# Optimization experiments

Hardware: AMD Instinct MI355X
Metric: run time of the kernel (lower is better)

## Reference

```python
import jax, jax.numpy as jnp
import numpy as np

B, T, H, V, C = 8192, 40, 128, 4450, 102

def setup_inputs() -> dict:
    key = jax.random.key(0)
    ks = jax.random.split(key, 9)
    s = 1.0 / np.sqrt(H)
    return {
        "input_ids": jax.random.randint(ks[0], (B, T), 0, V, dtype=jnp.int64),
        "emb_c": jax.random.normal(ks[1], (V, H), jnp.float32),
        "emb_a": jax.random.normal(ks[2], (V, H), jnp.float32),
        "W_ih": jax.random.uniform(ks[3], (3 * H, H), jnp.float32, -s, s),
        "W_hh": jax.random.uniform(ks[4], (3 * H, H), jnp.float32, -s, s),
        "b_ih": jax.random.uniform(ks[5], (3 * H,), jnp.float32, -s, s),
        "b_hh": jax.random.uniform(ks[6], (3 * H,), jnp.float32, -s, s),
        "W_cls": jax.random.uniform(ks[7], (C, H), jnp.float32, -s, s),
        "b_cls": jax.random.uniform(ks[8], (C,), jnp.float32, -s, s),
    }

def _gru_scan(x_seq, W_ih, W_hh, b_ih, b_hh):
    # x_seq: [T, B, H]; PyTorch GRU gate order: r, z, n
    h0 = jnp.zeros((x_seq.shape[1], H), x_seq.dtype)
    def step(h, x):
        gi = x @ W_ih.T + b_ih          # [B, 3H]
        gh = h @ W_hh.T + b_hh          # [B, 3H]
        i_r, i_z, i_n = jnp.split(gi, 3, axis=-1)
        h_r, h_z, h_n = jnp.split(gh, 3, axis=-1)
        r = jax.nn.sigmoid(i_r + h_r)
        z = jax.nn.sigmoid(i_z + h_z)
        n = jnp.tanh(i_n + r * h_n)
        h_new = (1.0 - z) * n + z * h
        return h_new, h_new
    _, hs = jax.lax.scan(step, h0, x_seq)
    return hs                            # [T, B, H]

def reference(input_ids, emb_c, emb_a, W_ih, W_hh, b_ih, b_hh, W_cls, b_cls):
    x_a = emb_a[input_ids].transpose(1, 0, 2)   # [T, B, H]
    x_c = emb_c[input_ids].transpose(1, 0, 2)
    ha = _gru_scan(x_a, W_ih, W_hh, b_ih, b_hh).transpose(1, 0, 2)  # [B, T, H]
    hc = _gru_scan(x_c, W_ih, W_hh, b_ih, b_hh).transpose(1, 0, 2)
    matrix = jnp.einsum('bth,bsh->bts', ha, ha)  # [B, T, T]
    A = jax.nn.softmax(matrix, axis=1)           # Softmax(dim=1) over 3D
    attn = A.transpose(0, 2, 1)                  # [B, T, T]
    # bmm(hc^T [B,H,T], attn).transpose -> out[b,s,h] = sum_t hc[b,t,h]*attn[b,t,s]
    out = jnp.einsum('bth,bts->bsh', hc, attn)   # [B, T, H]
    logits = out.reshape(-1, H) @ W_cls.T + b_cls  # [B*T, C]
    return jax.nn.softmax(logits, axis=1)
```

## Files before the change

### kernel.cpp

```cpp
#include <hip/hip_runtime.h>
#include <hip/hip_bf16.h>

#define BB 8192
#define TT 40
#define HH 128
#define CC 102
#define VV 4450

typedef __attribute__((ext_vector_type(8))) short short8;
typedef __attribute__((ext_vector_type(4))) float f4;

__device__ __forceinline__ float sigmoidf_(float x) { return 1.f / (1.f + __expf(-x)); }
__device__ __forceinline__ float tanhf_(float x) { float e = __expf(2.f * x); return 1.f - 2.f / (e + 1.f); }

__device__ __forceinline__ unsigned short f2bf(float x) {
    union { float f; unsigned u; } v; v.f = x;
    unsigned r = v.u + 0x7FFFu + ((v.u >> 16) & 1u);
    return (unsigned short)(r >> 16);
}
__device__ __forceinline__ float bf2f(unsigned short h) {
    union { float f; unsigned u; } v; v.u = ((unsigned)h) << 16; return v.f;
}
__device__ __forceinline__ short8 u4s8(uint4 v) { return *(short8*)&v; }

#define MFMA16(acc, a, b) acc = __builtin_amdgcn_mfma_f32_16x16x32_bf16(a, b, acc, 0, 0, 0)

__global__ __launch_bounds__(256) void prep_bf16split(const float* __restrict__ W,
                                                      unsigned short* __restrict__ hi,
                                                      unsigned short* __restrict__ lo, int n) {
    int i = blockIdx.x * 256 + threadIdx.x;
    if (i < n) {
        float x = W[i];
        unsigned short h = f2bf(x);
        hi[i] = h;
        lo[i] = f2bf(x - bf2f(h));
    }
}

__global__ __launch_bounds__(256) void prep_wcls(const float* __restrict__ W,
                                                 unsigned short* __restrict__ hi,
                                                 unsigned short* __restrict__ lo) {
    int i = blockIdx.x * 256 + threadIdx.x;
    if (i < 112 * HH) {
        int r = i >> 7;
        float x = (r < CC) ? W[i] : 0.f;
        unsigned short h = f2bf(x);
        hi[i] = h;
        lo[i] = f2bf(x - bf2f(h));
    }
}

__global__ __launch_bounds__(256) void prep_G_mfma(
    const float* __restrict__ emb_a, const float* __restrict__ emb_c,
    const unsigned short* __restrict__ WihH, const unsigned short* __restrict__ WihL,
    const float* __restrict__ b_ih, const float* __restrict__ b_hh,
    float* __restrict__ G)
{
    __shared__ uint4 se[2][32][16];

    const int tid = threadIdx.x;
    const int src = blockIdx.y;
    const float* emb = src ? emb_c : emb_a;
    const int v0 = blockIdx.x * 32;

    const int lane = tid & 63;
    const int w = tid >> 6;
    const int mcol = lane & 15;
    const int quad = lane >> 4;

#pragma unroll
    for (int i = 0; i < 4; ++i) {
        int task = tid + 256 * i;
        int row = task >> 5, q = task & 31;
        int v = v0 + row;
        float4 x = make_float4(0.f, 0.f, 0.f, 0.f);
        if (v < VV) x = ((const float4*)(emb + (size_t)v * HH))[q];
        unsigned short h0 = f2bf(x.x), h1 = f2bf(x.y), h2 = f2bf(x.z), h3 = f2bf(x.w);
        unsigned short l0 = f2bf(x.x - bf2f(h0)), l1 = f2bf(x.y - bf2f(h1));
        unsigned short l2 = f2bf(x.z - bf2f(h2)), l3 = f2bf(x.w - bf2f(h3));
        uint2 Hw, Lw;
        Hw.x = (unsigned)h0 | ((unsigned)h1 << 16); Hw.y = (unsigned)h2 | ((unsigned)h3 << 16);
        Lw.x = (unsigned)l0 | ((unsigned)l1 << 16); Lw.y = (unsigned)l2 | ((unsigned)l3 << 16);
        int phys = (q >> 1) ^ (row & 15);
        ((uint2*)&se[0][row][phys])[q & 1] = Hw;
        ((uint2*)&se[1][row][phys])[q & 1] = Lw;
    }

    float bias[6];
#pragma unroll
    for (int n6 = 0; n6 < 6; ++n6) {
        int c = w * 96 + n6 * 16 + mcol;
        bias[n6] = b_ih[c] + (c < 256 ? b_hh[c] : 0.f);
    }

    f4 acc[2][6];
#pragma unroll
    for (int mt = 0; mt < 2; ++mt)
#pragma unroll
        for (int n6 = 0; n6 < 6; ++n6) acc[mt][n6] = (f4){0.f, 0.f, 0.f, 0.f};

    __syncthreads();

#pragma unroll
    for (int kk = 0; kk < 4; ++kk) {
        uint4 bH[6], bL[6];
#pragma unroll
        for (int n6 = 0; n6 < 6; ++n6) {
            int rowc = w * 96 + n6 * 16 + mcol;
            bH[n6] = *((const uint4*)WihH + rowc * 16 + kk * 4 + quad);
            bL[n6] = *((const uint4*)WihL + rowc * 16 + kk * 4 + quad);
        }
#pragma unroll
        for (int mt = 0; mt < 2; ++mt) {
            int m = mt * 16 + mcol;
            int phys = (kk * 4 + quad) ^ mcol;
            short8 ah = u4s8(se[0][m][phys]);
            short8 al = u4s8(se[1][m][phys]);
#pragma unroll
            for (int n6 = 0; n6 < 6; ++n6) {
                MFMA16(acc[mt][n6], ah, u4s8(bH[n6]));
                MFMA16(acc[mt][n6], ah, u4s8(bL[n6]));
                MFMA16(acc[mt][n6], al, u4s8(bH[n6]));
            }
        }
    }

    float* gout = G + (size_t)src * VV * 384;
#pragma unroll
    for (int mt = 0; mt < 2; ++mt)
#pragma unroll
        for (int r = 0; r < 4; ++r) {
            int m = mt * 16 + quad * 4 + r;
            int v = v0 + m;
            if (v < VV) {
#pragma unroll
                for (int n6 = 0; n6 < 6; ++n6) {
                    int c = w * 96 + n6 * 16 + mcol;
                    gout[(size_t)v * 384 + c] = acc[mt][n6][r] + bias[n6];
                }
            }
        }
}

__global__ __launch_bounds__(512, 2) void gru_mfma(
    const int* __restrict__ ids, const float* __restrict__ G,
    const __hip_bfloat16* __restrict__ Whi, const __hip_bfloat16* __restrict__ Wlo,
    const float* __restrict__ b_hh, float* __restrict__ ha, float* __restrict__ hc)
{
    __shared__ uint4 sh[2][2][32][16];
    __shared__ int sids[32 * TT];

    const int tid = threadIdx.x;
    const int src = blockIdx.y;
    const int b0 = blockIdx.x * 32;
    const float* Gs = G + (size_t)src * VV * 384;
    float* hout = src ? hc : ha;

    const int lane = tid & 63;
    const int w = tid >> 6;
    const int nc0 = w * 16;
    const int mcol = lane & 15;
    const int quad = lane >> 4;

    for (int idx = tid; idx < 32 * TT; idx += 512)
        sids[idx] = ids[b0 * TT + idx];

    {
        uint4 z; z.x = z.y = z.z = z.w = 0u;
        uint4* p = &sh[0][0][0][0];
        for (int idx = tid; idx < 2 * 32 * 16; idx += 512) p[idx] = z;
    }

    short8 bh[3][4], bl[3][4];
#pragma unroll
    for (int g = 0; g < 3; ++g)
#pragma unroll
        for (int kk = 0; kk < 4; ++kk) {
            int row = g * 128 + nc0 + mcol;
            uint4 vh = *((const uint4*)Whi + row * 16 + kk * 4 + quad);
            uint4 vl = *((const uint4*)Wlo + row * 16 + kk * 4 + quad);
            bh[g][kk] = u4s8(vh);
            bl[g][kk] = u4s8(vl);
        }

    const float bhn = b_hh[256 + nc0 + mcol];
    const float* gbase = Gs + nc0 + mcol;

    f4 hreg[2];
    hreg[0] = (f4){0.f, 0.f, 0.f, 0.f};
    hreg[1] = (f4){0.f, 0.f, 0.f, 0.f};

    __syncthreads();

    float gc[3][2][4];
#pragma unroll
    for (int mt = 0; mt < 2; ++mt)
#pragma unroll
        for (int reg = 0; reg < 4; ++reg) {
            int m = mt * 16 + quad * 4 + reg;
            int id = sids[m * TT + 0];
            const float* gp = gbase + (size_t)id * 384;
            gc[0][mt][reg] = gp[0];
            gc[1][mt][reg] = gp[128];
            gc[2][mt][reg] = gp[256];
        }

    int buf = 0;
#pragma unroll 1
    for (int t = 0; t < TT; ++t) {
        f4 acc[3][2];
#pragma unroll
        for (int g = 0; g < 3; ++g)
#pragma unroll
            for (int mt = 0; mt < 2; ++mt) acc[g][mt] = (f4){0.f, 0.f, 0.f, 0.f};

#pragma unroll
        for (int mt = 0; mt < 2; ++mt)
#pragma unroll
            for (int kk = 0; kk < 4; ++kk) {
                int m = mt * 16 + mcol;
                int phys = (kk * 4 + quad) ^ mcol;
                uint4 avh = sh[buf][0][m][phys];
                uint4 avl = sh[buf][1][m][phys];
                short8 ah = u4s8(avh), al = u4s8(avl);
#pragma unroll
                for (int g = 0; g < 3; ++g) {
                    MFMA16(acc[g][mt], ah, bh[g][kk]);
                    MFMA16(acc[g][mt], ah, bl[g][kk]);
                    MFMA16(acc[g][mt], al, bh[g][kk]);
                }
            }

        const int nbuf = buf ^ 1;
        const int j = nc0 + mcol;
        const int s_slot = j >> 3;
        const int jb = j & 7;
#pragma unroll
        for (int mt = 0; mt < 2; ++mt) {
#pragma unroll
            for (int reg = 0; reg < 4; ++reg) {
                float rr = sigmoidf_(acc[0][mt][reg] + gc[0][mt][reg]);
                float zz = sigmoidf_(acc[1][mt][reg] + gc[1][mt][reg]);
                float nn = tanhf_(gc[2][mt][reg] + rr * (acc[2][mt][reg] + bhn));
                float hv = (1.f - zz) * nn + zz * hreg[mt][reg];
                hreg[mt][reg] = hv;

                int m = mt * 16 + quad * 4 + reg;
                hout[((size_t)(b0 + m) * TT + t) * HH + j] = hv;

                unsigned short hb = f2bf(hv);
                unsigned short lb = f2bf(hv - bf2f(hb));
                int phys = s_slot ^ (m & 15);
                ((unsigned short*)&sh[nbuf][0][m][phys])[jb] = hb;
                ((unsigned short*)&sh[nbuf][1][m][phys])[jb] = lb;
            }
        }

        if (t < TT - 1) {
#pragma unroll
            for (int mt = 0; mt < 2; ++mt)
#pragma unroll
                for (int reg = 0; reg < 4; ++reg) {
                    int m = mt * 16 + quad * 4 + reg;
                    int id = sids[m * TT + t + 1];
                    const float* gp = gbase + (size_t)id * 384;
                    gc[0][mt][reg] = gp[0];
                    gc[1][mt][reg] = gp[128];
                    gc[2][mt][reg] = gp[256];
                }
        }
        __syncthreads();
        buf ^= 1;
    }
}

#define AT_SHA     0
#define AT_SHA_LO  12288
#define AT_SHCT    24576
#define AT_SHCT_LO 40960
#define AT_SM      57344
#define AT_SW      66752
#define AT_SW_LO   72896
#define AT_PARTM   79040
#define AT_PARTD   79808
#define AT_SMX     80576
#define AT_SDI     80768
#define AT_TOTAL   80960

__global__ __launch_bounds__(256, 2) void attn_cls_mfma(
    const float* __restrict__ ha, const float* __restrict__ hc,
    const unsigned short* __restrict__ WcH, const unsigned short* __restrict__ WcL,
    const float* __restrict__ b_cls, float* __restrict__ out)
{
    __shared__ __attribute__((aligned(16))) char smem[AT_TOTAL];
    const int tid = threadIdx.x;
    const int lane = tid & 63;
    const int w = tid >> 6;
    const int quad = lane >> 4;
    const int col = lane & 15;
    const size_t b = blockIdx.x;

    float* sm    = (float*)(smem + AT_SM);
    float* slog  = (float*)(smem + AT_SM);
    float* partM = (float*)(smem + AT_PARTM);
    float* partD = (float*)(smem + AT_PARTD);
    float* sMX   = (float*)(smem + AT_SMX);
    float* sDI   = (float*)(smem + AT_SDI);

    const int ntc0 = (w < 3) ? w : 3;
    const int ntc1 = (w < 3) ? w + 4 : 3;
    uint4 bw[2][4][2];
    float bcv[2];
    {
        int nts[2] = {ntc0, ntc1};
#pragma unroll
        for (int which = 0; which < 2; ++which) {
            int row = nts[which] * 16 + col;
#pragma unroll
            for (int kk = 0; kk < 4; ++kk) {
                bw[which][kk][0] = *((const uint4*)WcH + row * 16 + kk * 4 + quad);
                bw[which][kk][1] = *((const uint4*)WcL + row * 16 + kk * 4 + quad);
            }
            bcv[which] = (row < CC) ? b_cls[row] : 0.f;
        }
    }

    {
        const float4* hab = (const float4*)(ha + b * TT * HH);
#pragma unroll
        for (int i = 0; i < 5; ++i) {
            int f4i = tid + 256 * i;
            int row = f4i >> 5, q = f4i & 31;
            float4 v = hab[f4i];
            unsigned short h0 = f2bf(v.x), h1 = f2bf(v.y), h2 = f2bf(v.z), h3 = f2bf(v.w);
            unsigned short l0 = f2bf(v.x - bf2f(h0)), l1 = f2bf(v.y - bf2f(h1));
            unsigned short l2 = f2bf(v.z - bf2f(h2)), l3 = f2bf(v.w - bf2f(h3));
            uint2 Hw, Lw;
            Hw.x = (unsigned)h0 | ((unsigned)h1 << 16); Hw.y = (unsigned)h2 | ((unsigned)h3 << 16);
            Lw.x = (unsigned)l0 | ((unsigned)l1 << 16); Lw.y = (unsigned)l2 | ((unsigned)l3 << 16);
            int phys = (q >> 1) ^ (row & 15);
            int off = row * 256 + phys * 16 + (q & 1) * 8;
            *(uint2*)(smem + AT_SHA + off) = Hw;
            *(uint2*)(smem + AT_SHA_LO + off) = Lw;
        }
        if (tid < 128) {
            int row = 40 + (tid >> 4), c = tid & 15;
            uint4 z; z.x = z.y = z.z = z.w = 0u;
            *(uint4*)(smem + AT_SHA + row * 256 + c * 16) = z;
            *(uint4*)(smem + AT_SHA_LO + row * 256 + c * 16) = z;
        }
        const float* hcb = hc + b * TT * HH;
        for (int task = tid; task < 640; task += 256) {
            int h = task & 127, c = task >> 7;
            unsigned short H8[8], L8[8];
#pragma unroll
            for (int jj = 0; jj < 8; ++jj) {
                float x = hcb[(c * 8 + jj) * HH + h];
                H8[jj] = f2bf(x);
                L8[jj] = f2bf(x - bf2f(H8[jj]));
            }
            uint4 Hq, Lq;
            Hq.x = (unsigned)H8[0] | ((unsigned)H8[1] << 16); Hq.y = (unsigned)H8[2] | ((unsigned)H8[3] << 16);
            Hq.z = (unsigned)H8[4] | ((unsigned)H8[5] << 16); Hq.w = (unsigned)H8[6] | ((unsigned)H8[7] << 16);
            Lq.x = (unsigned)L8[0] | ((unsigned)L8[1] << 16); Lq.y = (unsigned)L8[2] | ((unsigned)L8[3] << 16);
            Lq.z = (unsigned)L8[4] | ((unsigned)L8[5] << 16); Lq.w = (unsigned)L8[6] | ((unsigned)L8[7] << 16);
            int phys = c ^ (h & 7);
            *(uint4*)(smem + AT_SHCT + h * 128 + phys * 16) = Hq;
            *(uint4*)(smem + AT_SHCT_LO + h * 128 + phys * 16) = Lq;
        }
        for (int task = tid; task < 384; task += 256) {
            int h = task & 127, c = 5 + (task >> 7);
            int phys = c ^ (h & 7);
            uint4 z; z.x = z.y = z.z = z.w = 0u;
            *(uint4*)(smem + AT_SHCT + h * 128 + phys * 16) = z;
            *(uint4*)(smem + AT_SHCT_LO + h * 128 + phys * 16) = z;
        }
    }
    __syncthreads();

    if (w < 3) {
        const int mt = w;
        uint4 aH[4], aL[4];
#pragma unroll
        for (int kk = 0; kk < 4; ++kk) {
            int phys = (kk * 4 + quad) ^ col;
            int off = (mt * 16 + col) * 256 + phys * 16;
            aH[kk] = *(uint4*)(smem + AT_SHA + off);
            aL[kk] = *(uint4*)(smem + AT_SHA_LO + off);
        }
        f4 acc[3];
#pragma unroll
        for (int nt = 0; nt < 3; ++nt) acc[nt] = (f4){0.f, 0.f, 0.f, 0.f};
#pragma unroll
        for (int kk = 0; kk < 4; ++kk) {
            short8 ah = u4s8(aH[kk]), al = u4s8(aL[kk]);
#pragma unroll
            for (int nt = 0; nt < 3; ++nt) {
                int phys = (kk * 4 + quad) ^ col;
                int off = (nt * 16 + col) * 256 + phys * 16;
                short8 bH = u4s8(*(uint4*)(smem + AT_SHA + off));
                short8 bL = u4s8(*(uint4*)(smem + AT_SHA_LO + off));
                MFMA16(acc[nt], ah, bH);
                MFMA16(acc[nt], ah, bL);
                MFMA16(acc[nt], al, bH);
            }
        }
#pragma unroll
        for (int nt = 0; nt < 3; ++nt)
#pragma unroll
            for (int r = 0; r < 4; ++r)
                sm[(mt * 16 + quad * 4 + r) * 49 + nt * 16 + col] = acc[nt][r];
    }
    __syncthreads();

    if (tid < 160) {
        int t = tid >> 2, p = tid & 3;
        const float* row = sm + t * 49 + p * 10;
        float M = row[0];
#pragma unroll
        for (int i = 1; i < 10; ++i) M = fmaxf(M, row[i]);
        float D = 0.f;
#pragma unroll
        for (int i = 0; i < 10; ++i) D += __expf(row[i] - M);
        partM[t * 4 + p] = M;
        partD[t * 4 + p] = D;
    }
    __syncthreads();
    if (tid < 40) {
        float M = partM[tid * 4];
        M = fmaxf(M, partM[tid * 4 + 1]); M = fmaxf(M, partM[tid * 4 + 2]); M = fmaxf(M, partM[tid * 4 + 3]);
        float D = 0.f;
#pragma unroll
        for (int p = 0; p < 4; ++p) D += partD[tid * 4 + p] * __expf(partM[tid * 4 + p] - M);
        sMX[tid] = M;
        sDI[tid] = 1.f / D;
    }
    __syncthreads();

    for (int task = tid; task < 384; task += 256) {
        int s = task >> 3, c = task & 7;
        uint4 Hq, Lq;
        if (c >= 5) {
            Hq.x = Hq.y = Hq.z = Hq.w = 0u; Lq = Hq;
        } else {
            const float* srow = sm + s * 49 + c * 8;
            unsigned short H8[8], L8[8];
#pragma unroll
            for (int jj = 0; jj < 8; ++jj) {
                int t = c * 8 + jj;
                float wv = __expf(srow[jj] - sMX[t]) * sDI[t];
                H8[jj] = f2bf(wv);
                L8[jj] = f2bf(wv - bf2f(H8[jj]));
            }
            Hq.x = (unsigned)H8[0] | ((unsigned)H8[1] << 16); Hq.y = (unsigned)H8[2] | ((unsigned)H8[3] << 16);
            Hq.z = (unsigned)H8[4] | ((unsigned)H8[5] << 16); Hq.w = (unsigned)H8[6] | ((unsigned)H8[7] << 16);
            Lq.x = (unsigned)L8[0] | ((unsigned)L8[1] << 16); Lq.y = (unsigned)L8[2] | ((unsigned)L8[3] << 16);
            Lq.z = (unsigned)L8[4] | ((unsigned)L8[5] << 16); Lq.w = (unsigned)L8[6] | ((unsigned)L8[7] << 16);
        }
        int phys = c ^ (s & 7);
        *(uint4*)(smem + AT_SW + s * 128 + phys * 16) = Hq;
        *(uint4*)(smem + AT_SW_LO + s * 128 + phys * 16) = Lq;
    }
    __syncthreads();

    {
        uint4 aH[3][2], aL[3][2];
#pragma unroll
        for (int mt = 0; mt < 3; ++mt)
#pragma unroll
            for (int kk = 0; kk < 2; ++kk) {
                int s = mt * 16 + col;
                int phys = (kk * 4 + quad) ^ (s & 7);
                aH[mt][kk] = *(uint4*)(smem + AT_SW + s * 128 + phys * 16);
                aL[mt][kk] = *(uint4*)(smem + AT_SW_LO + s * 128 + phys * 16);
            }
        f4 acc[3][2];
#pragma unroll
        for (int mt = 0; mt < 3; ++mt) { acc[mt][0] = (f4){0,0,0,0}; acc[mt][1] = (f4){0,0,0,0}; }
#pragma unroll
        for (int which = 0; which < 2; ++which) {
            int nt = w + which * 4;
            int hrow = nt * 16 + col;
#pragma unroll
            for (int kk = 0; kk < 2; ++kk) {
                int phys = (kk * 4 + quad) ^ (hrow & 7);
                short8 bH = u4s8(*(uint4*)(smem + AT_SHCT + hrow * 128 + phys * 16));
                short8 bL = u4s8(*(uint4*)(smem + AT_SHCT_LO + hrow * 128 + phys * 16));
#pragma unroll
                for (int mt = 0; mt < 3; ++mt) {
                    short8 ah = u4s8(aH[mt][kk]), al = u4s8(aL[mt][kk]);
                    MFMA16(acc[mt][which], ah, bH);
                    MFMA16(acc[mt][which], ah, bL);
                    MFMA16(acc[mt][which], al, bH);
                }
            }
        }
        __syncthreads();
#pragma unroll
        for (int which = 0; which < 2; ++which) {
            int h = (w + which * 4) * 16 + col;
            int chunk = h >> 3, hb7 = (h & 7) * 2;
#pragma unroll
            for (int mt = 0; mt < 3; ++mt)
#pragma unroll
                for (int r = 0; r < 4; ++r) {
                    float v = acc[mt][which][r];
                    int s = mt * 16 + quad * 4 + r;
                    unsigned short hbv = f2bf(v);
                    unsigned short lbv = f2bf(v - bf2f(hbv));
                    int phys = chunk ^ (s & 15);
                    *(unsigned short*)(smem + AT_SHA + s * 256 + phys * 16 + hb7) = hbv;
                    *(unsigned short*)(smem + AT_SHA_LO + s * 256 + phys * 16 + hb7) = lbv;
                }
        }
    }
    __syncthreads();

    {
        f4 acc[3][2];
#pragma unroll
        for (int mt = 0; mt < 3; ++mt) { acc[mt][0] = (f4){0,0,0,0}; acc[mt][1] = (f4){0,0,0,0}; }
#pragma unroll
        for (int kk = 0; kk < 4; ++kk)
#pragma unroll
            for (int mt = 0; mt < 3; ++mt) {
                int s = mt * 16 + col;
                int phys = (kk * 4 + quad) ^ (s & 15);
                short8 ah = u4s8(*(uint4*)(smem + AT_SHA + s * 256 + phys * 16));
                short8 al = u4s8(*(uint4*)(smem + AT_SHA_LO + s * 256 + phys * 16));
#pragma unroll
                for (int which = 0; which < 2; ++which) {
                    MFMA16(acc[mt][which], ah, u4s8(bw[which][kk][0]));
                    MFMA16(acc[mt][which], ah, u4s8(bw[which][kk][1]));
                    MFMA16(acc[mt][which], al, u4s8(bw[which][kk][0]));
                }
            }
        __syncthreads();
        int nts[2] = {ntc0, ntc1};
#pragma unroll
        for (int which = 0; which < 2; ++which) {
            int c = nts[which] * 16 + col;
#pragma unroll
            for (int mt = 0; mt < 3; ++mt)
#pragma unroll
                for (int r = 0; r < 4; ++r)
                    slog[(mt * 16 + quad * 4 + r) * 113 + c] = acc[mt][which][r] + bcv[which];
        }
    }
    __syncthreads();

    if (tid < 160) {
        int s = tid >> 2, p = tid & 3;
        int c0 = p * 26;
        int c1 = (c0 + 26 < CC) ? c0 + 26 : CC;
        const float* row = slog + s * 113;
        float M = row[c0];
        for (int c = c0 + 1; c < c1; ++c) M = fmaxf(M, row[c]);
        float D = 0.f;
        for (int c = c0; c < c1; ++c) D += __expf(row[c] - M);
        partM[s * 4 + p] = M;
        partD[s * 4 + p] = D;
    }
    __syncthreads();
    if (tid < 40) {
        float M = partM[tid * 4];
        M = fmaxf(M, partM[tid * 4 + 1]); M = fmaxf(M, partM[tid * 4 + 2]); M = fmaxf(M, partM[tid * 4 + 3]);
        float D = 0.f;
#pragma unroll
        for (int p = 0; p < 4; ++p) D += partD[tid * 4 + p] * __expf(partM[tid * 4 + p] - M);
        sMX[tid] = M;
        sDI[tid] = 1.f / D;
    }
    __syncthreads();

    {
        int c = tid & 127, s0 = tid >> 7;
        if (c < CC) {
            float* ob = out + b * TT * CC;
            for (int s = s0; s < TT; s += 2)
                ob[s * CC + c] = __expf(slog[s * 113 + c] - sMX[s]) * sDI[s];
        }
    }
}

extern "C" void kernel_launch(void* const* d_in, const int* in_sizes, int n_in,
                              void* d_out, int out_size, void* d_ws, size_t ws_size,
                              hipStream_t stream) {
    const int*   ids   = (const int*)d_in[0];
    const float* emb_c = (const float*)d_in[1];
    const float* emb_a = (const float*)d_in[2];
    const float* W_ih  = (const float*)d_in[3];
    const float* W_hh  = (const float*)d_in[4];
    const float* b_ih  = (const float*)d_in[5];
    const float* b_hh  = (const float*)d_in[6];
    const float* W_cls = (const float*)d_in[7];
    const float* b_cls = (const float*)d_in[8];
    float* out = (float*)d_out;

    float* ha = (float*)d_ws;
    float* hc = ha + (size_t)BB * TT * HH;
    float* G  = hc + (size_t)BB * TT * HH;
    __hip_bfloat16* Whi = (__hip_bfloat16*)(G + (size_t)2 * VV * 384);
    __hip_bfloat16* Wlo = Whi + 384 * HH;
    unsigned short* WcH = (unsigned short*)(Wlo + 384 * HH);
    unsigned short* WcL = WcH + 112 * HH;
    unsigned short* WihH = WcL + 112 * HH;
    unsigned short* WihL = WihH + 384 * HH;

    prep_bf16split<<<(384 * HH + 255) / 256, 256, 0, stream>>>(W_hh, (unsigned short*)Whi, (unsigned short*)Wlo, 384 * HH);
    prep_bf16split<<<(384 * HH + 255) / 256, 256, 0, stream>>>(W_ih, WihH, WihL, 384 * HH);
    prep_wcls<<<(112 * HH + 255) / 256, 256, 0, stream>>>(W_cls, WcH, WcL);
    prep_G_mfma<<<dim3((VV + 31) / 32, 2), 256, 0, stream>>>(emb_a, emb_c, WihH, WihL, b_ih, b_hh, G);
    gru_mfma<<<dim3(BB / 32, 2), 512, 0, stream>>>(ids, G, Whi, Wlo, b_hh, ha, hc);
    attn_cls_mfma<<<BB, 256, 0, stream>>>(ha, hc, WcH, WcL, b_cls, out);
}
```

Before: 641.9 us.

## Use hardware bf16 pack conversion, fast reciprocals, interleaved gate table, higher GRU occupancy

Replaces the software round-to-nearest bf16 hi/lo split with the v_cvt_pk_bf16_f32 instruction across all kernels, and swaps IEEE divisions for hardware reciprocal in the sigmoid, tanh and softmax normalisers. The precomputed input-gate table is re-laid out so the r, z, n values for each hidden unit sit next to each other, letting the GRU step fetch them as one 12-byte load instead of three strided loads. The GRU kernel's launch bounds now ask for 4 blocks per CU, which caps register use and may cause spills given the weight fragments held in registers. Fast reciprocal slightly lowers accuracy.

```diff
diff --git a/kernel.cpp b/kernel.cpp
--- a/kernel.cpp
+++ b/kernel.cpp
@@ -10,8 +10,9 @@
 typedef __attribute__((ext_vector_type(8))) short short8;
 typedef __attribute__((ext_vector_type(4))) float f4;
 
-__device__ __forceinline__ float sigmoidf_(float x) { return 1.f / (1.f + __expf(-x)); }
-__device__ __forceinline__ float tanhf_(float x) { float e = __expf(2.f * x); return 1.f - 2.f / (e + 1.f); }
+__device__ __forceinline__ float rcpf_(float x) { return __builtin_amdgcn_rcpf(x); }
+__device__ __forceinline__ float sigmoidf_(float x) { return rcpf_(1.f + __expf(-x)); }
+__device__ __forceinline__ float tanhf_(float x) { float e = __expf(2.f * x); return 1.f - 2.f * rcpf_(e + 1.f); }
 
 __device__ __forceinline__ unsigned short f2bf(float x) {
     union { float f; unsigned u; } v; v.f = x;
@@ -22,6 +23,20 @@
     union { float f; unsigned u; } v; v.u = ((unsigned)h) << 16; return v.f;
 }
 __device__ __forceinline__ short8 u4s8(uint4 v) { return *(short8*)&v; }
+
+__device__ __forceinline__ unsigned cvtpk_bf16(float lo, float hi) {
+    unsigned r;
+    asm("v_cvt_pk_bf16_f32 %0, %1, %2" : "=v"(r) : "v"(lo), "v"(hi));
+    return r;
+}
+__device__ __forceinline__ void split2(float a, float b, unsigned& H, unsigned& L) {
+    H = cvtpk_bf16(a, b);
+    float ra = __uint_as_float(H << 16);
+    float rb = __uint_as_float(H & 0xFFFF0000u);
+    L = cvtpk_bf16(a - ra, b - rb);
+}
+
+struct __attribute__((aligned(4))) G3 { float r, z, n; };
 
 #define MFMA16(acc, a, b) acc = __builtin_amdgcn_mfma_f32_16x16x32_bf16(a, b, acc, 0, 0, 0)
 
@@ -75,12 +90,9 @@
         int v = v0 + row;
         float4 x = make_float4(0.f, 0.f, 0.f, 0.f);
         if (v < VV) x = ((const float4*)(emb + (size_t)v * HH))[q];
-        unsigned short h0 = f2bf(x.x), h1 = f2bf(x.y), h2 = f2bf(x.z), h3 = f2bf(x.w);
-        unsigned short l0 = f2bf(x.x - bf2f(h0)), l1 = f2bf(x.y - bf2f(h1));
-        unsigned short l2 = f2bf(x.z - bf2f(h2)), l3 = f2bf(x.w - bf2f(h3));
         uint2 Hw, Lw;
-        Hw.x = (unsigned)h0 | ((unsigned)h1 << 16); Hw.y = (unsigned)h2 | ((unsigned)h3 << 16);
-        Lw.x = (unsigned)l0 | ((unsigned)l1 << 16); Lw.y = (unsigned)l2 | ((unsigned)l3 << 16);
+        split2(x.x, x.y, Hw.x, Lw.x);
+        split2(x.z, x.w, Hw.y, Lw.y);
         int phys = (q >> 1) ^ (row & 15);
         ((uint2*)&se[0][row][phys])[q & 1] = Hw;
         ((uint2*)&se[1][row][phys])[q & 1] = Lw;
@@ -136,13 +148,14 @@
 #pragma unroll
                 for (int n6 = 0; n6 < 6; ++n6) {
                     int c = w * 96 + n6 * 16 + mcol;
-                    gout[(size_t)v * 384 + c] = acc[mt][n6][r] + bias[n6];
+                    int g = c >> 7, j = c & 127;
+                    gout[(size_t)v * 384 + j * 3 + g] = acc[mt][n6][r] + bias[n6];
                 }
             }
         }
 }
 
-__global__ __launch_bounds__(512, 2) void gru_mfma(
+__global__ __launch_bounds__(512, 4) void gru_mfma(
     const int* __restrict__ ids, const float* __restrict__ G,
     const __hip_bfloat16* __restrict__ Whi, const __hip_bfloat16* __restrict__ Wlo,
     const float* __restrict__ b_hh, float* __restrict__ ha, float* __restrict__ hc)
@@ -183,8 +196,9 @@
             bl[g][kk] = u4s8(vl);
         }
 
-    const float bhn = b_hh[256 + nc0 + mcol];
-    const float* gbase = Gs + nc0 + mcol;
+    const int j = nc0 + mcol;
+    const float bhn = b_hh[256 + j];
+    const float* gbase = Gs + 3 * j;
 
     f4 hreg[2];
     hreg[0] = (f4){0.f, 0.f, 0.f, 0.f};
@@ -192,18 +206,18 @@
 
     __syncthreads();
 
-    float gc[3][2][4];
+    G3 gc[2][4];
 #pragma unroll
     for (int mt = 0; mt < 2; ++mt)
 #pragma unroll
         for (int reg = 0; reg < 4; ++reg) {
             int m = mt * 16 + quad * 4 + reg;
             int id = sids[m * TT + 0];
-            const float* gp = gbase + (size_t)id * 384;
-            gc[0][mt][reg] = gp[0];
-            gc[1][mt][reg] = gp[128];
-            gc[2][mt][reg] = gp[256];
-        }
+            gc[mt][reg] = *(const G3*)(gbase + (size_t)id * 384);
+        }
+
+    const int s_slot = j >> 3;
+    const int jb = j & 7;
 
     int buf = 0;
 #pragma unroll 1
@@ -232,27 +246,35 @@
             }
 
         const int nbuf = buf ^ 1;
-        const int j = nc0 + mcol;
-        const int s_slot = j >> 3;
-        const int jb = j & 7;
 #pragma unroll
         for (int mt = 0; mt < 2; ++mt) {
+            float hv4[4];
 #pragma unroll
             for (int reg = 0; reg < 4; ++reg) {
-                float rr = sigmoidf_(acc[0][mt][reg] + gc[0][mt][reg]);
-                float zz = sigmoidf_(acc[1][mt][reg] + gc[1][mt][reg]);
-                float nn = tanhf_(gc[2][mt][reg] + rr * (acc[2][mt][reg] + bhn));
-                float hv = (1.f - zz) * nn + zz * hreg[mt][reg];
+                G3 g = gc[mt][reg];
+                float rr = sigmoidf_(acc[0][mt][reg] + g.r);
+                float zz = sigmoidf_(acc[1][mt][reg] + g.z);
+                float nn = tanhf_(g.n + rr * (acc[2][mt][reg] + bhn));
+                float hv = fmaf(zz, hreg[mt][reg] - nn, nn);
                 hreg[mt][reg] = hv;
+                hv4[reg] = hv;
 
                 int m = mt * 16 + quad * 4 + reg;
                 hout[((size_t)(b0 + m) * TT + t) * HH + j] = hv;
-
-                unsigned short hb = f2bf(hv);
-                unsigned short lb = f2bf(hv - bf2f(hb));
-                int phys = s_slot ^ (m & 15);
-                ((unsigned short*)&sh[nbuf][0][m][phys])[jb] = hb;
-                ((unsigned short*)&sh[nbuf][1][m][phys])[jb] = lb;
+            }
+#pragma unroll
+            for (int pr = 0; pr < 2; ++pr) {
+                unsigned Hp, Lp;
+                split2(hv4[pr * 2], hv4[pr * 2 + 1], Hp, Lp);
+#pragma unroll
+                for (int k = 0; k < 2; ++k) {
+                    int m = mt * 16 + quad * 4 + pr * 2 + k;
+                    int phys = s_slot ^ (m & 15);
+                    unsigned short hb = (unsigned short)(k ? (Hp >> 16) : Hp);
+                    unsigned short lb = (unsigned short)(k ? (Lp >> 16) : Lp);
+                    ((unsigned short*)&sh[nbuf][0][m][phys])[jb] = hb;
+                    ((unsigned short*)&sh[nbuf][1][m][phys])[jb] = lb;
+                }
             }
         }
 
@@ -263,10 +285,7 @@
                 for (int reg = 0; reg < 4; ++reg) {
                     int m = mt * 16 + quad * 4 + reg;
                     int id = sids[m * TT + t + 1];
-                    const float* gp = gbase + (size_t)id * 384;
-                    gc[0][mt][reg] = gp[0];
-                    gc[1][mt][reg] = gp[128];
-                    gc[2][mt][reg] = gp[256];
+                    gc[mt][reg] = *(const G3*)(gbase + (size_t)id * 384);
                 }
         }
         __syncthreads();
@@ -332,12 +351,9 @@
             int f4i = tid + 256 * i;
             int row = f4i >> 5, q = f4i & 31;
             float4 v = hab[f4i];
-            unsigned short h0 = f2bf(v.x), h1 = f2bf(v.y), h2 = f2bf(v.z), h3 = f2bf(v.w);
-            unsigned short l0 = f2bf(v.x - bf2f(h0)), l1 = f2bf(v.y - bf2f(h1));
-            unsigned short l2 = f2bf(v.z - bf2f(h2)), l3 = f2bf(v.w - bf2f(h3));
             uint2 Hw, Lw;
-            Hw.x = (unsigned)h0 | ((unsigned)h1 << 16); Hw.y = (unsigned)h2 | ((unsigned)h3 << 16);
-            Lw.x = (unsigned)l0 | ((unsigned)l1 << 16); Lw.y = (unsigned)l2 | ((unsigned)l3 << 16);
+            split2(v.x, v.y, Hw.x, Lw.x);
+            split2(v.z, v.w, Hw.y, Lw.y);
             int phys = (q >> 1) ^ (row & 15);
             int off = row * 256 + phys * 16 + (q & 1) * 8;
             *(uint2*)(smem + AT_SHA + off) = Hw;
@@ -352,18 +368,14 @@
         const float* hcb = hc + b * TT * HH;
         for (int task = tid; task < 640; task += 256) {
             int h = task & 127, c = task >> 7;
-            unsigned short H8[8], L8[8];
-#pragma unroll
-            for (int jj = 0; jj < 8; ++jj) {
-                float x = hcb[(c * 8 + jj) * HH + h];
-                H8[jj] = f2bf(x);
-                L8[jj] = f2bf(x - bf2f(H8[jj]));
-            }
+            float x[8];
+#pragma unroll
+            for (int jj = 0; jj < 8; ++jj) x[jj] = hcb[(c * 8 + jj) * HH + h];
             uint4 Hq, Lq;
-            Hq.x = (unsigned)H8[0] | ((unsigned)H8[1] << 16); Hq.y = (unsigned)H8[2] | ((unsigned)H8[3] << 16);
-            Hq.z = (unsigned)H8[4] | ((unsigned)H8[5] << 16); Hq.w = (unsigned)H8[6] | ((unsigned)H8[7] << 16);
-            Lq.x = (unsigned)L8[0] | ((unsigned)L8[1] << 16); Lq.y = (unsigned)L8[2] | ((unsigned)L8[3] << 16);
-            Lq.z = (unsigned)L8[4] | ((unsigned)L8[5] << 16); Lq.w = (unsigned)L8[6] | ((unsigned)L8[7] << 16);
+            split2(x[0], x[1], Hq.x, Lq.x);
+            split2(x[2], x[3], Hq.y, Lq.y);
+            split2(x[4], x[5], Hq.z, Lq.z);
+            split2(x[6], x[7], Hq.w, Lq.w);
             int phys = c ^ (h & 7);
             *(uint4*)(smem + AT_SHCT + h * 128 + phys * 16) = Hq;
             *(uint4*)(smem + AT_SHCT_LO + h * 128 + phys * 16) = Lq;
@@ -433,7 +445,7 @@
 #pragma unroll
         for (int p = 0; p < 4; ++p) D += partD[tid * 4 + p] * __expf(partM[tid * 4 + p] - M);
         sMX[tid] = M;
-        sDI[tid] = 1.f / D;
+        sDI[tid] = rcpf_(D);
     }
     __syncthreads();
 
@@ -444,18 +456,16 @@
             Hq.x = Hq.y = Hq.z = Hq.w = 0u; Lq = Hq;
         } else {
             const float* srow = sm + s * 49 + c * 8;
-            unsigned short H8[8], L8[8];
+            float wv[8];
 #pragma unroll
             for (int jj = 0; jj < 8; ++jj) {
                 int t = c * 8 + jj;
-                float wv = __expf(srow[jj] - sMX[t]) * sDI[t];
-                H8[jj] = f2bf(wv);
-                L8[jj] = f2bf(wv - bf2f(H8[jj]));
-            }
-            Hq.x = (unsigned)H8[0] | ((unsigned)H8[1] << 16); Hq.y = (unsigned)H8[2] | ((unsigned)H8[3] << 16);
-            Hq.z = (unsigned)H8[4] | ((unsigned)H8[5] << 16); Hq.w = (unsigned)H8[6] | ((unsigned)H8[7] << 16);
-            Lq.x = (unsigned)L8[0] | ((unsigned)L8[1] << 16); Lq.y = (unsigned)L8[2] | ((unsigned)L8[3] << 16);
-            Lq.z = (unsigned)L8[4] | ((unsigned)L8[5] << 16); Lq.w = (unsigned)L8[6] | ((unsigned)L8[7] << 16);
+                wv[jj] = __expf(srow[jj] - sMX[t]) * sDI[t];
+            }
+            split2(wv[0], wv[1], Hq.x, Lq.x);
+            split2(wv[2], wv[3], Hq.y, Lq.y);
+            split2(wv[4], wv[5], Hq.z, Lq.z);
+            split2(wv[6], wv[7], Hq.w, Lq.w);
         }
         int phys = c ^ (s & 7);
         *(uint4*)(smem + AT_SW + s * 128 + phys * 16) = Hq;
@@ -503,14 +513,18 @@
 #pragma unroll
             for (int mt = 0; mt < 3; ++mt)
 #pragma unroll
-                for (int r = 0; r < 4; ++r) {
-                    float v = acc[mt][which][r];
-                    int s = mt * 16 + quad * 4 + r;
-                    unsigned short hbv = f2bf(v);
-                    unsigned short lbv = f2bf(v - bf2f(hbv));
-                    int phys = chunk ^ (s & 15);
-                    *(unsigned short*)(smem + AT_SHA + s * 256 + phys * 16 + hb7) = hbv;
-                    *(unsigned short*)(smem + AT_SHA_LO + s * 256 + phys * 16 + hb7) = lbv;
+                for (int pr = 0; pr < 2; ++pr) {
+                    unsigned Hp, Lp;
+                    split2(acc[mt][which][pr * 2], acc[mt][which][pr * 2 + 1], Hp, Lp);
+#pragma unroll
+                    for (int k = 0; k < 2; ++k) {
+                        int s = mt * 16 + quad * 4 + pr * 2 + k;
+                        int phys = chunk ^ (s & 15);
+                        *(unsigned short*)(smem + AT_SHA + s * 256 + phys * 16 + hb7) =
+                            (unsigned short)(k ? (Hp >> 16) : Hp);
+                        *(unsigned short*)(smem + AT_SHA_LO + s * 256 + phys * 16 + hb7) =
+                            (unsigned short)(k ? (Lp >> 16) : Lp);
+                    }
                 }
         }
     }
@@ -569,7 +583,7 @@
 #pragma unroll
         for (int p = 0; p < 4; ++p) D += partD[tid * 4 + p] * __expf(partM[tid * 4 + p] - M);
         sMX[tid] = M;
-        sDI[tid] = 1.f / D;
+        sDI[tid] = rcpf_(D);
     }
     __syncthreads();
 
```

Result: slower. 1.716 ms (+167.4%).
